# Kernel optimization log

Measured on AMD Instinct MI355X. Metric: run time of the kernel, lower is better.

Reference implementation:

```python
import jax, jax.numpy as jnp
import numpy as np

C = 64            # number of classes (all assumed present in y)
NUM_OVERLAP = 64  # int(args.d * args.overlap_ratio) = int(256 * 0.25)
ALPHA = 1.0       # args.alpha


def setup_inputs() -> dict:
    key = jax.random.key(0)
    k1, k2 = jax.random.split(key)
    x = jax.random.normal(k1, (65536, 512), dtype=jnp.float32)
    y = jax.random.randint(k2, (65536,), 0, C)
    return {"x": x, "y": y}


def reference(x, y):
    # one-hot class membership [C, N]
    member = (y[None, :] == jnp.arange(C)[:, None])
    counts = member.sum(axis=1).astype(x.dtype)                    # [C]
    # class centers: mean of member rows -> [C, D]
    centers = (member.astype(x.dtype) @ x) / counts[:, None]
    # pairwise L2 distance from every center to every sample, [C, N],
    # via ||c||^2 + ||x||^2 - 2 c.x (avoids [C, N, D] intermediate)
    c2 = jnp.sum(centers * centers, axis=1)[:, None]               # [C, 1]
    x2 = jnp.sum(x * x, axis=1)[None, :]                           # [1, N]
    d2 = c2 + x2 - 2.0 * (centers @ x.T)                           # [C, N]
    dist = jnp.sqrt(jnp.maximum(d2, 1e-12))
    neg_inf = jnp.asarray(-jnp.inf, dist.dtype)
    # positives: largest NUM_OVERLAP distances among same-class samples
    pos_vals = jax.lax.top_k(jnp.where(member, dist, neg_inf), NUM_OVERLAP)[0]
    pos_mean = pos_vals.mean(axis=1)                               # [C]
    # negatives: smallest NUM_OVERLAP distances among other-class samples
    neg_vals = -jax.lax.top_k(jnp.where(member, neg_inf, -dist), NUM_OVERLAP)[0]
    neg_mean = neg_vals.mean(axis=1)                               # [C]
    per_class = jnp.maximum(ALPHA + pos_mean - neg_mean, 0.0)
    loss = jnp.sum(per_class) / (C * NUM_OVERLAP)
    return loss.reshape(1)
```

## Files before the change

kernel.cpp:

```cpp
#include <hip/hip_runtime.h>
#include <hip/hip_bf16.h>
#include <math.h>

#define N_SAMP 65536
#define DIM    512
#define NCLS   64
#define KSEL   64
#define SNBIN  4096

#define OFF_COUNTS   0u
#define OFF_CSUM     256u
#define OFF_CENTERS  131328u
#define OFF_C2       196864u
#define OFF_MEANS    197120u
#define OFF_DONE     197632u
#define OFF_DIST     262144u

typedef __attribute__((ext_vector_type(8))) short bf16x8;
typedef __attribute__((ext_vector_type(4))) float f32x4;

__device__ __forceinline__ unsigned short f2bf_rne(float f) {
  const unsigned u = __float_as_uint(f);
  return (unsigned short)((u + 0x7FFFu + ((u >> 16) & 1u)) >> 16);
}

__global__ __launch_bounds__(256) void k_init(int* __restrict__ counts,
                                              float* __restrict__ csum,
                                              unsigned* __restrict__ done) {
  const int i = blockIdx.x * 256 + threadIdx.x;
  const int stride = gridDim.x * 256;
  if (i < NCLS) counts[i] = 0;
  if (i == 0) *done = 0u;
  for (int j = i; j < NCLS * DIM; j += stride) csum[j] = 0.f;
}

__global__ __launch_bounds__(256) void k_class_sums(const float* __restrict__ x,
                                                    const int* __restrict__ y,
                                                    float* __restrict__ csum,
                                                    int* __restrict__ counts) {
  __shared__ int list[4096];
  __shared__ int lcnt;
  const int c  = blockIdx.x >> 4;
  const int r0 = (blockIdx.x & 15) * 4096;
  const int tid = threadIdx.x;
  if (tid == 0) lcnt = 0;
  __syncthreads();
  for (int i = tid; i < 4096; i += 256) {
    if (y[r0 + i] == c) { int p = atomicAdd(&lcnt, 1); list[p] = r0 + i; }
  }
  __syncthreads();
  const int n = lcnt;
  const int dbase = (tid >> 6) * 128 + (tid & 63) * 2;
  float a0 = 0.f, a1 = 0.f, b0 = 0.f, b1 = 0.f;
  int i = 0;
  for (; i + 2 <= n; i += 2) {
    const float* p0 = x + (size_t)list[i] * DIM + dbase;
    const float* p1 = x + (size_t)list[i + 1] * DIM + dbase;
    a0 += p0[0]; a1 += p0[1];
    b0 += p1[0]; b1 += p1[1];
  }
  if (i < n) { const float* p0 = x + (size_t)list[i] * DIM + dbase; a0 += p0[0]; a1 += p0[1]; }
  a0 += b0; a1 += b1;
  atomicAdd(&csum[c * DIM + dbase], a0);
  atomicAdd(&csum[c * DIM + dbase + 1], a1);
  if (tid == 0) atomicAdd(&counts[c], n);
}

__global__ __launch_bounds__(64) void k_centers(const float* __restrict__ csum,
                                                const int* __restrict__ counts,
                                                unsigned short* __restrict__ cenb,
                                                float* __restrict__ c2) {
  const int c = blockIdx.x, l = threadIdx.x;
  const float inv = 1.0f / (float)counts[c];
  float ss = 0.f;
  #pragma unroll
  for (int j = 0; j < 8; ++j) {
    int d = j * 64 + l;
    float v = csum[c * DIM + d] * inv;
    cenb[c * DIM + d] = f2bf_rne(v);
    ss += v * v;
  }
  #pragma unroll
  for (int o = 32; o; o >>= 1) ss += __shfl_down(ss, o, 64);
  if (l == 0) c2[c] = ss;
}

#define CSTR 520
__global__ __launch_bounds__(512, 4) void k_dist_mfma(const float* __restrict__ x,
                                                      const unsigned short* __restrict__ cenb,
                                                      const float* __restrict__ c2,
                                                      float* __restrict__ dist) {
  __shared__ unsigned short cenS[NCLS * CSTR];
  __shared__ float c2s[NCLS];

  const int tid = threadIdx.x;
  const int wave = tid >> 6;
  const int lane = tid & 63;
  const int s0 = blockIdx.x * 128 + wave * 16;
  const int samp = s0 + (lane & 15);
  const int kg = lane >> 4;

  for (int q = tid; q < 4096; q += 512) {
    const int row = q >> 6, cc = q & 63;
    const uint4 v = *reinterpret_cast<const uint4*>(cenb + row * DIM + cc * 8);
    *reinterpret_cast<uint4*>(&cenS[row * CSTR + cc * 8]) = v;
  }
  if (tid < NCLS) c2s[tid] = c2[tid];
  __syncthreads();

  f32x4 acc[4] = {f32x4{0,0,0,0}, f32x4{0,0,0,0}, f32x4{0,0,0,0}, f32x4{0,0,0,0}};
  float x2 = 0.f;
  const float* __restrict__ xrow = x + (size_t)samp * DIM + kg * 8;
  const int arow = lane & 15;

  union BB { bf16x8 v; __hip_bfloat162 h[4]; };

  #pragma unroll 4
  for (int s = 0; s < 16; ++s) {
    const int k0 = s * 32;
    float xf[8];
    *reinterpret_cast<float4*>(&xf[0]) = *reinterpret_cast<const float4*>(xrow + k0);
    *reinterpret_cast<float4*>(&xf[4]) = *reinterpret_cast<const float4*>(xrow + k0 + 4);
    BB bb;
    bb.h[0] = __float22bfloat162_rn(make_float2(xf[0], xf[1]));
    bb.h[1] = __float22bfloat162_rn(make_float2(xf[2], xf[3]));
    bb.h[2] = __float22bfloat162_rn(make_float2(xf[4], xf[5]));
    bb.h[3] = __float22bfloat162_rn(make_float2(xf[6], xf[7]));
    #pragma unroll
    for (int j = 0; j < 8; ++j) x2 = fmaf(xf[j], xf[j], x2);
    const int kidx = k0 + kg * 8;
    const bf16x8 a0 = *reinterpret_cast<const bf16x8*>(&cenS[(arow +  0) * CSTR + kidx]);
    const bf16x8 a1 = *reinterpret_cast<const bf16x8*>(&cenS[(arow + 16) * CSTR + kidx]);
    const bf16x8 a2 = *reinterpret_cast<const bf16x8*>(&cenS[(arow + 32) * CSTR + kidx]);
    const bf16x8 a3 = *reinterpret_cast<const bf16x8*>(&cenS[(arow + 48) * CSTR + kidx]);
    acc[0] = __builtin_amdgcn_mfma_f32_16x16x32_bf16(a0, bb.v, acc[0], 0, 0, 0);
    acc[1] = __builtin_amdgcn_mfma_f32_16x16x32_bf16(a1, bb.v, acc[1], 0, 0, 0);
    acc[2] = __builtin_amdgcn_mfma_f32_16x16x32_bf16(a2, bb.v, acc[2], 0, 0, 0);
    acc[3] = __builtin_amdgcn_mfma_f32_16x16x32_bf16(a3, bb.v, acc[3], 0, 0, 0);
  }

  x2 += __shfl_xor(x2, 16, 64);
  x2 += __shfl_xor(x2, 32, 64);

  const int col = s0 + (lane & 15);
  #pragma unroll
  for (int t = 0; t < 4; ++t) {
    #pragma unroll
    for (int r = 0; r < 4; ++r) {
      const int cls = t * 16 + (lane >> 4) * 4 + r;
      const float d2 = c2s[cls] + x2 - 2.0f * acc[t][r];
      dist[(size_t)cls * N_SAMP + col] = sqrtf(fmaxf(d2, 1e-12f));
    }
  }
}

__device__ __forceinline__ void redB(float v0, float v2, float v3, float* redf, float* bcast) {
  #pragma unroll
  for (int o = 32; o; o >>= 1) {
    v0 += __shfl_xor(v0, o, 64);
    v2 = fminf(v2, __shfl_xor(v2, o, 64));
    v3 = fmaxf(v3, __shfl_xor(v3, o, 64));
  }
  const int wid = threadIdx.x >> 6;
  if ((threadIdx.x & 63) == 0) { redf[wid] = v0; redf[16 + wid] = v2; redf[32 + wid] = v3; }
  __syncthreads();
  if (threadIdx.x < 16) {
    const int l = threadIdx.x;
    float a0 = redf[l], a2 = redf[16 + l], a3 = redf[32 + l];
    #pragma unroll
    for (int o = 8; o; o >>= 1) {
      a0 += __shfl_xor(a0, o, 64);
      a2 = fminf(a2, __shfl_xor(a2, o, 64));
      a3 = fmaxf(a3, __shfl_xor(a3, o, 64));
    }
    if (l == 0) { bcast[0] = a0; bcast[2] = a2; bcast[3] = a3; }
  }
  __syncthreads();
}

__device__ __forceinline__ int binS(float w, float lo, float sc) {
  int b = (int)((w - lo) * sc);
  b = b < SNBIN - 1 ? b : SNBIN - 1;
  return b > 0 ? b : 0;
}

__device__ __forceinline__ float wavePeel(const float* buf, int cnt, int need, int lane) {
  float thr = -1e30f, s = 0.f;
  int taken = 0;
  for (int g = 0; g < 64 && taken < need; ++g) {
    float m = 1e30f;
    for (int t = 0; t < 16; ++t) {
      const int idx = lane + t * 64;
      if (idx < cnt) { const float u = buf[idx]; if (u > thr) m = fminf(m, u); }
    }
    #pragma unroll
    for (int o = 32; o; o >>= 1) m = fminf(m, __shfl_xor(m, o, 64));
    int ce = 0;
    for (int t = 0; t < 16; ++t) {
      const int idx = lane + t * 64;
      if (idx < cnt && buf[idx] == m) ++ce;
    }
    #pragma unroll
    for (int o = 32; o; o >>= 1) ce += __shfl_xor(ce, o, 64);
    const int take = (need - taken) < ce ? (need - taken) : ce;
    s += (float)take * m;
    taken += take;
    thr = m;
  }
  return s;
}

__global__ __launch_bounds__(1024, 2) void k_select4(const float* __restrict__ dist,
                                                     const int* __restrict__ y,
                                                     float* __restrict__ means,
                                                     unsigned* __restrict__ done,
                                                     float* __restrict__ out) {
  __shared__ unsigned bitmap[2048];
  __shared__ unsigned hist[SNBIN];
  __shared__ unsigned wscan[16];
  __shared__ float redf[48];
  __shared__ float bcast[4];
  __shared__ float bbuf[1024];
  __shared__ int bcnt_s, bsel_s;
  __shared__ unsigned strict_s;
  __shared__ float bsum_s;
  __shared__ int lastflag;

  const int tid = threadIdx.x;
  const int lane = tid & 63;
  const int wid = tid >> 6;
  const int c = blockIdx.x >> 1;
  const int role = blockIdx.x & 1;
  const float* __restrict__ row = dist + (size_t)c * N_SAMP;

  if (tid == 0) { bcnt_s = 0; bsel_s = 0; strict_s = 0u; bsum_s = 0.f; lastflag = 0; }

  {
    const int4* __restrict__ y4 = (const int4*)(y + tid * 64);
    unsigned w0 = 0u, w1 = 0u;
    #pragma unroll
    for (int i = 0; i < 8; ++i) {
      const int4 a = y4[i];
      w0 |= (unsigned)(a.x == c) << (i * 4);
      w0 |= (unsigned)(a.y == c) << (i * 4 + 1);
      w0 |= (unsigned)(a.z == c) << (i * 4 + 2);
      w0 |= (unsigned)(a.w == c) << (i * 4 + 3);
    }
    #pragma unroll
    for (int i = 0; i < 8; ++i) {
      const int4 a = y4[8 + i];
      w1 |= (unsigned)(a.x == c) << (i * 4);
      w1 |= (unsigned)(a.y == c) << (i * 4 + 1);
      w1 |= (unsigned)(a.z == c) << (i * 4 + 2);
      w1 |= (unsigned)(a.w == c) << (i * 4 + 3);
    }
    bitmap[tid * 2] = w0;
    bitmap[tid * 2 + 1] = w1;
  }
  __syncthreads();

  float mn = 1e30f, mx = -1e30f;
  #pragma unroll 4
  for (int i = 0; i < 16; ++i) {
    const int base = i * 4096 + tid * 4;
    const float4 v4 = *reinterpret_cast<const float4*>(row + base);
    const unsigned bits = bitmap[base >> 5] >> (base & 31);
    const float vv[4] = {v4.x, v4.y, v4.z, v4.w};
    #pragma unroll
    for (int j = 0; j < 4; ++j) {
      if ((int)((bits >> j) & 1u) != role) {
        const float w = role ? vv[j] : -vv[j];
        mn = fminf(mn, w);
        mx = fmaxf(mx, w);
      }
    }
  }
  redB(0.f, mn, mx, redf, bcast);
  const float lo = bcast[2], hi = bcast[3];
  const bool deg = !(hi > lo);
  float meanval;

  if (deg) {
    meanval = role ? lo : -lo;
  } else {
    const float sc = (float)SNBIN / (hi - lo);
    for (int i = tid; i < SNBIN; i += 1024) hist[i] = 0u;
    __syncthreads();

    #pragma unroll 4
    for (int i = 0; i < 16; ++i) {
      const int base = i * 4096 + tid * 4;
      const float4 v4 = *reinterpret_cast<const float4*>(row + base);
      const unsigned bits = bitmap[base >> 5] >> (base & 31);
      const float vv[4] = {v4.x, v4.y, v4.z, v4.w};
      #pragma unroll
      for (int j = 0; j < 4; ++j) {
        if ((int)((bits >> j) & 1u) != role) {
          const float w = role ? vv[j] : -vv[j];
          atomicAdd(&hist[binS(w, lo, sc)], 1u);
        }
      }
    }
    __syncthreads();

    {
      unsigned b4[4]; unsigned s4 = 0;
      #pragma unroll
      for (int j = 0; j < 4; ++j) { b4[j] = hist[tid * 4 + j]; s4 += b4[j]; }
      unsigned cum = s4;
      #pragma unroll
      for (int d = 1; d < 64; d <<= 1) {
        const unsigned t = (unsigned)__shfl_up((int)cum, d, 64);
        if (lane >= d) cum += t;
      }
      if (lane == 63) wscan[wid] = cum;
      __syncthreads();
      if (tid < 16) {
        unsigned v = wscan[tid];
        #pragma unroll
        for (int d = 1; d < 16; d <<= 1) {
          const unsigned t = (unsigned)__shfl_up((int)v, d, 64);
          if (tid >= d) v += t;
        }
        wscan[tid] = v;
      }
      __syncthreads();
      const unsigned gcum = cum + (wid ? wscan[wid - 1] : 0u);
      const unsigned gprev = gcum - s4;
      if (gcum >= (unsigned)KSEL && gprev < (unsigned)KSEL) {
        unsigned run = gprev;
        #pragma unroll
        for (int j = 0; j < 4; ++j) {
          if (run + b4[j] >= (unsigned)KSEL) { bsel_s = tid * 4 + j; strict_s = run; break; }
          run += b4[j];
        }
      }
      __syncthreads();
    }
    const int B = bsel_s;
    const int need = KSEL - (int)strict_s;

    float ss = 0.f;
    #pragma unroll 4
    for (int i = 0; i < 16; ++i) {
      const int base = i * 4096 + tid * 4;
      const float4 v4 = *reinterpret_cast<const float4*>(row + base);
      const unsigned bits = bitmap[base >> 5] >> (base & 31);
      const float vv[4] = {v4.x, v4.y, v4.z, v4.w};
      #pragma unroll
      for (int j = 0; j < 4; ++j) {
        if ((int)((bits >> j) & 1u) != role) {
          const float w = role ? vv[j] : -vv[j];
          const int b = binS(w, lo, sc);
          if (b < B) ss += w;
          else if (b == B) { const int p = atomicAdd(&bcnt_s, 1); if (p < 1024) bbuf[p] = w; }
        }
      }
    }
    redB(ss, 0.f, 0.f, redf, bcast);
    const float SS = bcast[0];
    const int cnt = bcnt_s;

    if (cnt <= 1024) {
      if (wid == 0) {
        const float s = wavePeel(bbuf, cnt, need, lane);
        if (lane == 0) bsum_s = s;
      }
      __syncthreads();
    } else {
      float thr = -1e30f, accum = 0.f;
      int taken = 0;
      for (int g = 0; g < 64 && taken < need; ++g) {
        float m = 1e30f;
        for (int i = 0; i < 16; ++i) {
          const int base = i * 4096 + tid * 4;
          const float4 v4 = *reinterpret_cast<const float4*>(row + base);
          const unsigned bits = bitmap[base >> 5] >> (base & 31);
          const float vv[4] = {v4.x, v4.y, v4.z, v4.w};
          for (int j = 0; j < 4; ++j) {
            if ((int)((bits >> j) & 1u) != role) {
              const float w = role ? vv[j] : -vv[j];
              if (binS(w, lo, sc) == B && w > thr) m = fminf(m, w);
            }
          }
        }
        redB(0.f, m, 0.f, redf, bcast);
        const float M = bcast[2];
        float ce = 0.f;
        for (int i = 0; i < 16; ++i) {
          const int base = i * 4096 + tid * 4;
          const float4 v4 = *reinterpret_cast<const float4*>(row + base);
          const unsigned bits = bitmap[base >> 5] >> (base & 31);
          const float vv[4] = {v4.x, v4.y, v4.z, v4.w};
          for (int j = 0; j < 4; ++j) {
            if ((int)((bits >> j) & 1u) != role) {
              const float w = role ? vv[j] : -vv[j];
              if (w == M) ce += 1.f;
            }
          }
        }
        redB(ce, 0.f, 0.f, redf, bcast);
        const int CE = (int)bcast[0];
        const int take = (need - taken) < CE ? (need - taken) : CE;
        accum += (float)take * M;
        taken += take;
        thr = M;
      }
      if (tid == 0) bsum_s = accum;
      __syncthreads();
    }

    const float total = SS + bsum_s;
    meanval = role ? total * (1.0f / 64.0f) : -total * (1.0f / 64.0f);
  }

  if (tid == 0) {
    __hip_atomic_store(&means[role * 64 + c], meanval, __ATOMIC_RELAXED, __HIP_MEMORY_SCOPE_AGENT);
    const unsigned old = __hip_atomic_fetch_add(done, 1u, __ATOMIC_ACQ_REL, __HIP_MEMORY_SCOPE_AGENT);
    lastflag = (old == 127u) ? 1 : 0;
  }
  __syncthreads();
  if (lastflag && tid < 64) {
    const float pm = __hip_atomic_load(&means[tid], __ATOMIC_ACQUIRE, __HIP_MEMORY_SCOPE_AGENT);
    const float nm = __hip_atomic_load(&means[64 + tid], __ATOMIC_ACQUIRE, __HIP_MEMORY_SCOPE_AGENT);
    float pc = fmaxf(1.0f + pm - nm, 0.0f);
    #pragma unroll
    for (int o = 32; o; o >>= 1) pc += __shfl_down(pc, o, 64);
    if (tid == 0) out[0] = pc * (1.0f / 4096.0f);
  }
}

extern "C" void kernel_launch(void* const* d_in, const int* in_sizes, int n_in,
                              void* d_out, int out_size, void* d_ws, size_t ws_size,
                              hipStream_t stream) {
  const float* x = (const float*)d_in[0];
  const int* y = (const int*)d_in[1];
  float* out = (float*)d_out;
  char* w = (char*)d_ws;
  int* counts          = (int*)(w + OFF_COUNTS);
  float* csum          = (float*)(w + OFF_CSUM);
  unsigned short* cenb = (unsigned short*)(w + OFF_CENTERS);
  float* c2            = (float*)(w + OFF_C2);
  float* means         = (float*)(w + OFF_MEANS);
  unsigned* done       = (unsigned*)(w + OFF_DONE);
  float* dist          = (float*)(w + OFF_DIST);

  hipLaunchKernelGGL(k_init, dim3(64), dim3(256), 0, stream, counts, csum, done);
  hipLaunchKernelGGL(k_class_sums, dim3(1024), dim3(256), 0, stream, x, y, csum, counts);
  hipLaunchKernelGGL(k_centers, dim3(64), dim3(64), 0, stream, csum, counts, cenb, c2);
  hipLaunchKernelGGL(k_dist_mfma, dim3(N_SAMP / 128), dim3(512), 0, stream, x, cenb, c2, dist);
  hipLaunchKernelGGL(k_select4, dim3(128), dim3(1024), 0, stream, dist, y, means, done, out);
}
```

Baseline: 101.9 us.

## Replace per-class gather sums with LDS scatter partials and two-stage center reduction

The old per-class gather kernel re-scanned y for each class and read x with scattered rows, so x was read once per class chunk. The new k_accum reads each 256-row tile of x once and scatter-adds rows into a 64x512 LDS accumulator, then writes per-block partials. k_centers2 reduces those partials per class and chunk, and k_dist splits the centers staging into two K-halves to cut LDS and raise occupancy. This removes the init kernel and global atomics, but adds a 32 MB partial buffer written and read back, plus heavy LDS atomic contention.

Result: slower. 278.5 us (+173.1%).

```diff
diff --git a/kernel.cpp b/kernel.cpp
--- a/kernel.cpp
+++ b/kernel.cpp
@@ -8,13 +8,13 @@
 #define KSEL   64
 #define SNBIN  4096
 
-#define OFF_COUNTS   0u
-#define OFF_CSUM     256u
-#define OFF_CENTERS  131328u
-#define OFF_C2       196864u
-#define OFF_MEANS    197120u
-#define OFF_DONE     197632u
-#define OFF_DIST     262144u
+#define OFF_CENB    0u
+#define OFF_GC2P    65536u
+#define OFF_MEANS   67584u
+#define OFF_DONE    68096u
+#define OFF_GCOUNT  131072u
+#define OFF_DIST    262144u
+#define OFF_GPART   17039360u
 
 typedef __attribute__((ext_vector_type(8))) short bf16x8;
 typedef __attribute__((ext_vector_type(4))) float f32x4;
@@ -24,73 +24,100 @@
   return (unsigned short)((u + 0x7FFFu + ((u >> 16) & 1u)) >> 16);
 }
 
-__global__ __launch_bounds__(256) void k_init(int* __restrict__ counts,
-                                              float* __restrict__ csum,
-                                              unsigned* __restrict__ done) {
-  const int i = blockIdx.x * 256 + threadIdx.x;
-  const int stride = gridDim.x * 256;
-  if (i < NCLS) counts[i] = 0;
-  if (i == 0) *done = 0u;
-  for (int j = i; j < NCLS * DIM; j += stride) csum[j] = 0.f;
-}
-
-__global__ __launch_bounds__(256) void k_class_sums(const float* __restrict__ x,
-                                                    const int* __restrict__ y,
-                                                    float* __restrict__ csum,
-                                                    int* __restrict__ counts) {
-  __shared__ int list[4096];
-  __shared__ int lcnt;
-  const int c  = blockIdx.x >> 4;
-  const int r0 = (blockIdx.x & 15) * 4096;
+__global__ __launch_bounds__(512, 2) void k_accum(const float* __restrict__ x,
+                                                  const int* __restrict__ y,
+                                                  float* __restrict__ gpartial,
+                                                  int* __restrict__ gcount) {
+  __shared__ float accS[NCLS * DIM];
+  __shared__ int ycache[256];
+  __shared__ int hcnt[NCLS];
   const int tid = threadIdx.x;
-  if (tid == 0) lcnt = 0;
-  __syncthreads();
-  for (int i = tid; i < 4096; i += 256) {
-    if (y[r0 + i] == c) { int p = atomicAdd(&lcnt, 1); list[p] = r0 + i; }
-  }
-  __syncthreads();
-  const int n = lcnt;
-  const int dbase = (tid >> 6) * 128 + (tid & 63) * 2;
-  float a0 = 0.f, a1 = 0.f, b0 = 0.f, b1 = 0.f;
-  int i = 0;
-  for (; i + 2 <= n; i += 2) {
-    const float* p0 = x + (size_t)list[i] * DIM + dbase;
-    const float* p1 = x + (size_t)list[i + 1] * DIM + dbase;
-    a0 += p0[0]; a1 += p0[1];
-    b0 += p1[0]; b1 += p1[1];
-  }
-  if (i < n) { const float* p0 = x + (size_t)list[i] * DIM + dbase; a0 += p0[0]; a1 += p0[1]; }
-  a0 += b0; a1 += b1;
-  atomicAdd(&csum[c * DIM + dbase], a0);
-  atomicAdd(&csum[c * DIM + dbase + 1], a1);
-  if (tid == 0) atomicAdd(&counts[c], n);
-}
-
-__global__ __launch_bounds__(64) void k_centers(const float* __restrict__ csum,
-                                                const int* __restrict__ counts,
-                                                unsigned short* __restrict__ cenb,
-                                                float* __restrict__ c2) {
-  const int c = blockIdx.x, l = threadIdx.x;
-  const float inv = 1.0f / (float)counts[c];
-  float ss = 0.f;
-  #pragma unroll
-  for (int j = 0; j < 8; ++j) {
-    int d = j * 64 + l;
-    float v = csum[c * DIM + d] * inv;
-    cenb[c * DIM + d] = f2bf_rne(v);
-    ss += v * v;
-  }
-  #pragma unroll
-  for (int o = 32; o; o >>= 1) ss += __shfl_down(ss, o, 64);
-  if (l == 0) c2[c] = ss;
-}
-
-#define CSTR 520
-__global__ __launch_bounds__(512, 4) void k_dist_mfma(const float* __restrict__ x,
-                                                      const unsigned short* __restrict__ cenb,
-                                                      const float* __restrict__ c2,
-                                                      float* __restrict__ dist) {
-  __shared__ unsigned short cenS[NCLS * CSTR];
+  const int b = blockIdx.x;
+  const int row0 = b * 256;
+  const int g = tid >> 8;
+  const int t = tid & 255;
+
+  for (int i = tid; i < NCLS * DIM; i += 512) accS[i] = 0.f;
+  if (tid < NCLS) hcnt[tid] = 0;
+  if (tid < 256) ycache[tid] = y[row0 + tid];
+  __syncthreads();
+  if (tid < 256) atomicAdd(&hcnt[ycache[tid]], 1);
+
+  const int d0 = t * 2;
+  for (int i = 0; i < 128; i += 8) {
+    float2 v[8]; int cls[8];
+    #pragma unroll
+    for (int q = 0; q < 8; ++q) {
+      const int r = 2 * (i + q) + g;
+      cls[q] = ycache[r];
+      v[q] = *reinterpret_cast<const float2*>(x + (size_t)(row0 + r) * DIM + d0);
+    }
+    #pragma unroll
+    for (int q = 0; q < 8; ++q) {
+      atomicAdd(&accS[cls[q] * DIM + d0], v[q].x);
+      atomicAdd(&accS[cls[q] * DIM + d0 + 1], v[q].y);
+    }
+  }
+  __syncthreads();
+
+  float* __restrict__ dst = gpartial + (size_t)b * (NCLS * DIM);
+  for (int i = tid; i < NCLS * DIM; i += 512) dst[i] = accS[i];
+  if (tid < NCLS) gcount[b * NCLS + tid] = hcnt[tid];
+}
+
+__global__ __launch_bounds__(256) void k_centers2(const float* __restrict__ gpartial,
+                                                  const int* __restrict__ gcount,
+                                                  unsigned short* __restrict__ cenb,
+                                                  float* __restrict__ gc2p) {
+  __shared__ float redc[4][64];
+  __shared__ int cntS;
+  const int tid = threadIdx.x;
+  const int c = blockIdx.x >> 3;
+  const int chunk = blockIdx.x & 7;
+  const int j = tid & 63;
+  const int part = tid >> 6;
+
+  {
+    int cv = gcount[tid * NCLS + c];
+    #pragma unroll
+    for (int o = 32; o; o >>= 1) cv += __shfl_xor(cv, o, 64);
+    __shared__ int cw[4];
+    if ((tid & 63) == 0) cw[tid >> 6] = cv;
+    __syncthreads();
+    if (tid == 0) cntS = cw[0] + cw[1] + cw[2] + cw[3];
+    __syncthreads();
+  }
+
+  const size_t base = (size_t)c * DIM + chunk * 64 + j;
+  float s = 0.f;
+  for (int b = part; b < 256; b += 32) {
+    float t8[8];
+    #pragma unroll
+    for (int q = 0; q < 8; ++q)
+      t8[q] = gpartial[(size_t)(b + q * 4) * (NCLS * DIM) + base];
+    #pragma unroll
+    for (int q = 0; q < 8; ++q) s += t8[q];
+  }
+  redc[part][j] = s;
+  __syncthreads();
+  if (part == 0) {
+    const float total = redc[0][j] + redc[1][j] + redc[2][j] + redc[3][j];
+    const float center = total / (float)cntS;
+    cenb[base] = f2bf_rne(center);
+    float c2v = center * center;
+    #pragma unroll
+    for (int o = 32; o; o >>= 1) c2v += __shfl_xor(c2v, o, 64);
+    if (j == 0) gc2p[c * 8 + chunk] = c2v;
+  }
+}
+
+#define CSTR2 264
+__global__ __launch_bounds__(512, 6) void k_dist(const float* __restrict__ x,
+                                                 const unsigned short* __restrict__ cenb,
+                                                 const float* __restrict__ gc2p,
+                                                 float* __restrict__ dist,
+                                                 unsigned* __restrict__ done) {
+  __shared__ unsigned short cenS[NCLS * CSTR2];
   __shared__ float c2s[NCLS];
 
   const int tid = threadIdx.x;
@@ -99,44 +126,53 @@
   const int s0 = blockIdx.x * 128 + wave * 16;
   const int samp = s0 + (lane & 15);
   const int kg = lane >> 4;
-
-  for (int q = tid; q < 4096; q += 512) {
-    const int row = q >> 6, cc = q & 63;
-    const uint4 v = *reinterpret_cast<const uint4*>(cenb + row * DIM + cc * 8);
-    *reinterpret_cast<uint4*>(&cenS[row * CSTR + cc * 8]) = v;
-  }
-  if (tid < NCLS) c2s[tid] = c2[tid];
-  __syncthreads();
+  const int arow = lane & 15;
+
+  if (blockIdx.x == 0 && tid == 0) *done = 0u;
+  if (tid < NCLS) {
+    float s = 0.f;
+    #pragma unroll
+    for (int k = 0; k < 8; ++k) s += gc2p[tid * 8 + k];
+    c2s[tid] = s;
+  }
 
   f32x4 acc[4] = {f32x4{0,0,0,0}, f32x4{0,0,0,0}, f32x4{0,0,0,0}, f32x4{0,0,0,0}};
   float x2 = 0.f;
   const float* __restrict__ xrow = x + (size_t)samp * DIM + kg * 8;
-  const int arow = lane & 15;
-
   union BB { bf16x8 v; __hip_bfloat162 h[4]; };
 
-  #pragma unroll 4
-  for (int s = 0; s < 16; ++s) {
-    const int k0 = s * 32;
-    float xf[8];
-    *reinterpret_cast<float4*>(&xf[0]) = *reinterpret_cast<const float4*>(xrow + k0);
-    *reinterpret_cast<float4*>(&xf[4]) = *reinterpret_cast<const float4*>(xrow + k0 + 4);
-    BB bb;
-    bb.h[0] = __float22bfloat162_rn(make_float2(xf[0], xf[1]));
-    bb.h[1] = __float22bfloat162_rn(make_float2(xf[2], xf[3]));
-    bb.h[2] = __float22bfloat162_rn(make_float2(xf[4], xf[5]));
-    bb.h[3] = __float22bfloat162_rn(make_float2(xf[6], xf[7]));
-    #pragma unroll
-    for (int j = 0; j < 8; ++j) x2 = fmaf(xf[j], xf[j], x2);
-    const int kidx = k0 + kg * 8;
-    const bf16x8 a0 = *reinterpret_cast<const bf16x8*>(&cenS[(arow +  0) * CSTR + kidx]);
-    const bf16x8 a1 = *reinterpret_cast<const bf16x8*>(&cenS[(arow + 16) * CSTR + kidx]);
-    const bf16x8 a2 = *reinterpret_cast<const bf16x8*>(&cenS[(arow + 32) * CSTR + kidx]);
-    const bf16x8 a3 = *reinterpret_cast<const bf16x8*>(&cenS[(arow + 48) * CSTR + kidx]);
-    acc[0] = __builtin_amdgcn_mfma_f32_16x16x32_bf16(a0, bb.v, acc[0], 0, 0, 0);
-    acc[1] = __builtin_amdgcn_mfma_f32_16x16x32_bf16(a1, bb.v, acc[1], 0, 0, 0);
-    acc[2] = __builtin_amdgcn_mfma_f32_16x16x32_bf16(a2, bb.v, acc[2], 0, 0, 0);
-    acc[3] = __builtin_amdgcn_mfma_f32_16x16x32_bf16(a3, bb.v, acc[3], 0, 0, 0);
+  #pragma unroll
+  for (int half = 0; half < 2; ++half) {
+    __syncthreads();
+    for (int q = tid; q < 2048; q += 512) {
+      const int row = q >> 5, cc = q & 31;
+      const uint4 v = *reinterpret_cast<const uint4*>(cenb + row * DIM + half * 256 + cc * 8);
+      *reinterpret_cast<uint4*>(&cenS[row * CSTR2 + cc * 8]) = v;
+    }
+    __syncthreads();
+    #pragma unroll
+    for (int s = 0; s < 8; ++s) {
+      const int kglob = half * 256 + s * 32;
+      const int kloc = s * 32 + kg * 8;
+      float xf[8];
+      *reinterpret_cast<float4*>(&xf[0]) = *reinterpret_cast<const float4*>(xrow + kglob);
+      *reinterpret_cast<float4*>(&xf[4]) = *reinterpret_cast<const float4*>(xrow + kglob + 4);
+      BB bb;
+      bb.h[0] = __float22bfloat162_rn(make_float2(xf[0], xf[1]));
+      bb.h[1] = __float22bfloat162_rn(make_float2(xf[2], xf[3]));
+      bb.h[2] = __float22bfloat162_rn(make_float2(xf[4], xf[5]));
+      bb.h[3] = __float22bfloat162_rn(make_float2(xf[6], xf[7]));
+      #pragma unroll
+      for (int jj = 0; jj < 8; ++jj) x2 = fmaf(xf[jj], xf[jj], x2);
+      const bf16x8 a0 = *reinterpret_cast<const bf16x8*>(&cenS[(arow +  0) * CSTR2 + kloc]);
+      const bf16x8 a1 = *reinterpret_cast<const bf16x8*>(&cenS[(arow + 16) * CSTR2 + kloc]);
+      const bf16x8 a2 = *reinterpret_cast<const bf16x8*>(&cenS[(arow + 32) * CSTR2 + kloc]);
+      const bf16x8 a3 = *reinterpret_cast<const bf16x8*>(&cenS[(arow + 48) * CSTR2 + kloc]);
+      acc[0] = __builtin_amdgcn_mfma_f32_16x16x32_bf16(a0, bb.v, acc[0], 0, 0, 0);
+      acc[1] = __builtin_amdgcn_mfma_f32_16x16x32_bf16(a1, bb.v, acc[1], 0, 0, 0);
+      acc[2] = __builtin_amdgcn_mfma_f32_16x16x32_bf16(a2, bb.v, acc[2], 0, 0, 0);
+      acc[3] = __builtin_amdgcn_mfma_f32_16x16x32_bf16(a3, bb.v, acc[3], 0, 0, 0);
+    }
   }
 
   x2 += __shfl_xor(x2, 16, 64);
@@ -144,11 +180,11 @@
 
   const int col = s0 + (lane & 15);
   #pragma unroll
-  for (int t = 0; t < 4; ++t) {
+  for (int tq = 0; tq < 4; ++tq) {
     #pragma unroll
     for (int r = 0; r < 4; ++r) {
-      const int cls = t * 16 + (lane >> 4) * 4 + r;
-      const float d2 = c2s[cls] + x2 - 2.0f * acc[t][r];
+      const int cls = tq * 16 + (lane >> 4) * 4 + r;
+      const float d2 = c2s[cls] + x2 - 2.0f * acc[tq][r];
       dist[(size_t)cls * N_SAMP + col] = sqrtf(fmaxf(d2, 1e-12f));
     }
   }
@@ -437,17 +473,16 @@
   const int* y = (const int*)d_in[1];
   float* out = (float*)d_out;
   char* w = (char*)d_ws;
-  int* counts          = (int*)(w + OFF_COUNTS);
-  float* csum          = (float*)(w + OFF_CSUM);
-  unsigned short* cenb = (unsigned short*)(w + OFF_CENTERS);
-  float* c2            = (float*)(w + OFF_C2);
+  unsigned short* cenb = (unsigned short*)(w + OFF_CENB);
+  float* gc2p          = (float*)(w + OFF_GC2P);
   float* means         = (float*)(w + OFF_MEANS);
   unsigned* done       = (unsigned*)(w + OFF_DONE);
+  int* gcount          = (int*)(w + OFF_GCOUNT);
   float* dist          = (float*)(w + OFF_DIST);
-
-  hipLaunchKernelGGL(k_init, dim3(64), dim3(256), 0, stream, counts, csum, done);
-  hipLaunchKernelGGL(k_class_sums, dim3(1024), dim3(256), 0, stream, x, y, csum, counts);
-  hipLaunchKernelGGL(k_centers, dim3(64), dim3(64), 0, stream, csum, counts, cenb, c2);
-  hipLaunchKernelGGL(k_dist_mfma, dim3(N_SAMP / 128), dim3(512), 0, stream, x, cenb, c2, dist);
+  float* gpartial      = (float*)(w + OFF_GPART);
+
+  hipLaunchKernelGGL(k_accum, dim3(256), dim3(512), 0, stream, x, y, gpartial, gcount);
+  hipLaunchKernelGGL(k_centers2, dim3(512), dim3(256), 0, stream, gpartial, gcount, cenb, gc2p);
+  hipLaunchKernelGGL(k_dist, dim3(N_SAMP / 128), dim3(512), 0, stream, x, cenb, gc2p, dist, done);
   hipLaunchKernelGGL(k_select4, dim3(128), dim3(1024), 0, stream, dist, y, means, done, out);
 }
```
